# Kernel optimization log

Measured on AMD Instinct MI355X. Metric: run time of the kernel, lower is better.

## Reference

```python
import jax, jax.numpy as jnp
import numpy as np

N_NODES = 10000
N_EDGES = 80000
IN_DIM = 512
H1, H2, OUT_DIM = 4096, 1024, 7
NEG_SLOPE = 0.2


def _gat_layer(x, src, dst, W, a_src, a_dst, b, n_nodes):
    # x: [N, F_in] -> h: [N, F_out]
    h = x @ W
    # per-edge attention logits: a_src . h_i + a_dst . h_j (PyG GATConv, heads=1)
    e = jax.nn.leaky_relu((h @ a_src)[src] + (h @ a_dst)[dst], NEG_SLOPE)
    # segment softmax over destination nodes
    m = jax.ops.segment_max(e, dst, num_segments=n_nodes)
    ex = jnp.exp(e - m[dst])
    denom = jax.ops.segment_sum(ex, dst, num_segments=n_nodes)
    alpha = ex / denom[dst]
    # scatter-add weighted messages
    out = jax.ops.segment_sum(alpha[:, None] * h[src], dst, num_segments=n_nodes)
    return out + b


def setup_inputs() -> dict:
    key = jax.random.key(0)
    ks = jax.random.split(key, 16)
    s = 0.05
    inp = {
        "x": jax.random.normal(ks[0], (N_NODES, IN_DIM), dtype=jnp.float32),
        "edge_index": jax.random.randint(ks[1], (2, N_EDGES), 0, N_NODES, dtype=jnp.int32),
        "W1": jax.random.normal(ks[2], (IN_DIM, H1), dtype=jnp.float32) * s,
        "att_src1": jax.random.normal(ks[3], (H1,), dtype=jnp.float32) * s,
        "att_dst1": jax.random.normal(ks[4], (H1,), dtype=jnp.float32) * s,
        "b1": jnp.zeros((H1,), dtype=jnp.float32),
        "W2": jax.random.normal(ks[5], (H1, H2), dtype=jnp.float32) * s,
        "att_src2": jax.random.normal(ks[6], (H2,), dtype=jnp.float32) * s,
        "att_dst2": jax.random.normal(ks[7], (H2,), dtype=jnp.float32) * s,
        "b2": jnp.zeros((H2,), dtype=jnp.float32),
        "W3": jax.random.normal(ks[8], (H2, OUT_DIM), dtype=jnp.float32) * s,
        "att_src3": jax.random.normal(ks[9], (OUT_DIM,), dtype=jnp.float32) * s,
        "att_dst3": jax.random.normal(ks[10], (OUT_DIM,), dtype=jnp.float32) * s,
        "b3": jnp.zeros((OUT_DIM,), dtype=jnp.float32),
    }
    return inp


def reference(x, edge_index, W1, att_src1, att_dst1, b1,
              W2, att_src2, att_dst2, b2,
              W3, att_src3, att_dst3, b3):
    n = x.shape[0]
    loops = jnp.arange(n, dtype=edge_index.dtype)
    src = jnp.concatenate([edge_index[0], loops])  # add_self_loops=True
    dst = jnp.concatenate([edge_index[1], loops])
    h = _gat_layer(x, src, dst, W1, att_src1, att_dst1, b1, n)
    h = jax.nn.relu(h)  # dropout is identity in eval mode
    h = _gat_layer(h, src, dst, W2, att_src2, att_dst2, b2, n)
    h = jax.nn.relu(h)
    h = _gat_layer(h, src, dst, W3, att_src3, att_dst3, b3, n)
    return jax.nn.log_softmax(h, axis=1)
```

## Files before the change

kernel.cpp:

```cpp
#include <hip/hip_runtime.h>
#include <hip/hip_bf16.h>
#include <math.h>

#define NNODES  10000
#define NEDGES  80000
#define NTOT    90000
#define IN_DIM  512
#define H1_DIM  4096
#define H2_DIM  1024
#define ODIM    7
#define MAXDEG  128
#define NEG_SLOPE 0.2f

typedef __hip_bfloat16 bf16;
typedef __attribute__((ext_vector_type(8))) short short8;
typedef __attribute__((ext_vector_type(4))) float f32x4;

__device__ inline void unpack_bf2(unsigned u, float& lo, float& hi) {
    union { unsigned i; float f; } a, b;
    a.i = u << 16; b.i = u & 0xffff0000u;
    lo = a.f; hi = b.f;
}

#define ASYNC_COPY16(lds, g)                                                              \
    __builtin_amdgcn_global_load_lds((const __attribute__((address_space(1))) void*)(g),  \
                                     (__attribute__((address_space(3))) void*)(lds),      \
                                     16, 0, 0)

__global__ void build_bucket(const int* __restrict__ ei, int* cnt, int* bucket) {
    int k = blockIdx.x * blockDim.x + threadIdx.x;
    if (k >= NTOT) return;
    int s, d;
    if (k < NEDGES) { s = ei[k]; d = ei[NEDGES + k]; }
    else            { s = k - NEDGES; d = s; }
    int pos = atomicAdd(&cnt[d], 1);
    if (pos < MAXDEG) bucket[d * MAXDEG + pos] = s;
}

__global__ __launch_bounds__(256) void transpose_fold(const float* __restrict__ W,
                                                      bf16* __restrict__ WT,
                                                      const float* __restrict__ a_s,
                                                      const float* __restrict__ a_d,
                                                      float* __restrict__ w_s,
                                                      float* __restrict__ w_d,
                                                      int R, int C) {
    __shared__ float t[32][33];
    int c0 = blockIdx.x * 32, r0 = blockIdx.y * 32;
    int x = threadIdx.x & 31, y = threadIdx.x >> 5;
    float asv = a_s[c0 + x], adv = a_d[c0 + x];
    #pragma unroll
    for (int dy = 0; dy < 32; dy += 8) {
        float w = W[(size_t)(r0 + y + dy) * C + c0 + x];
        t[y + dy][x] = w;
        float ps = w * asv, pd = w * adv;
        #pragma unroll
        for (int off = 16; off > 0; off >>= 1) {
            ps += __shfl_down(ps, off, 32);
            pd += __shfl_down(pd, off, 32);
        }
        if (x == 0) {
            atomicAdd(&w_s[r0 + y + dy], ps);
            atomicAdd(&w_d[r0 + y + dy], pd);
        }
    }
    __syncthreads();
    #pragma unroll
    for (int dy = 0; dy < 32; dy += 8)
        WT[(size_t)(c0 + y + dy) * R + r0 + x] = __float2bfloat16(t[x][y + dy]);
}

__global__ __launch_bounds__(128) void dots_cvt1(const float* __restrict__ X,
                                                 const float* __restrict__ w_s,
                                                 const float* __restrict__ w_d,
                                                 float* __restrict__ s_src,
                                                 float* __restrict__ s_dst,
                                                 bf16* __restrict__ XB) {
    int n = blockIdx.x;
    int t = threadIdx.x;
    float4 xv = ((const float4*)(X + (size_t)n * IN_DIM))[t];
    float4 wsv = ((const float4*)w_s)[t];
    float4 wdv = ((const float4*)w_d)[t];
    bf16 o[4] = { __float2bfloat16(xv.x), __float2bfloat16(xv.y),
                  __float2bfloat16(xv.z), __float2bfloat16(xv.w) };
    *(uint2*)(XB + (size_t)n * IN_DIM + 4 * t) = *(uint2*)o;
    float ss = xv.x*wsv.x + xv.y*wsv.y + xv.z*wsv.z + xv.w*wsv.w;
    float sd = xv.x*wdv.x + xv.y*wdv.y + xv.z*wdv.z + xv.w*wdv.w;
    #pragma unroll
    for (int off = 32; off > 0; off >>= 1) {
        ss += __shfl_down(ss, off);
        sd += __shfl_down(sd, off);
    }
    __shared__ float red[2][2];
    int wave = t >> 6;
    if ((t & 63) == 0) { red[0][wave] = ss; red[1][wave] = sd; }
    __syncthreads();
    if (t == 0) {
        s_src[n] = red[0][0] + red[0][1];
        s_dst[n] = red[1][0] + red[1][1];
    }
}

__global__ __launch_bounds__(128) void agg1(const bf16* __restrict__ XB,
                                            const float* __restrict__ s_src,
                                            const float* __restrict__ s_dst,
                                            const int* __restrict__ bucket,
                                            const int* __restrict__ cnt,
                                            bf16* __restrict__ OUT) {
    int n = blockIdx.x;
    int c = min(cnt[n], MAXDEG);
    __shared__ float alpha[MAXDEG];
    __shared__ int   ssrc[MAXDEG];
    if (threadIdx.x < c) {
        int s = bucket[n * MAXDEG + threadIdx.x];
        ssrc[threadIdx.x] = s;
        float e = s_src[s] + s_dst[n];
        alpha[threadIdx.x] = (e > 0.f) ? e : NEG_SLOPE * e;
    }
    __syncthreads();
    if (threadIdx.x == 0) {
        float m = -1e30f;
        for (int j = 0; j < c; ++j) m = fmaxf(m, alpha[j]);
        float s = 0.f;
        for (int j = 0; j < c; ++j) { float ex = __expf(alpha[j] - m); alpha[j] = ex; s += ex; }
        float inv = 1.f / s;
        for (int j = 0; j < c; ++j) alpha[j] *= inv;
    }
    __syncthreads();
    int t = threadIdx.x;
    float acc[4] = {};
    for (int j = 0; j < c; ++j) {
        float a = alpha[j];
        uint2 raw = ((const uint2*)(XB + (size_t)ssrc[j] * IN_DIM))[t];
        float f0, f1, f2, f3;
        unpack_bf2(raw.x, f0, f1); unpack_bf2(raw.y, f2, f3);
        acc[0] = fmaf(a, f0, acc[0]); acc[1] = fmaf(a, f1, acc[1]);
        acc[2] = fmaf(a, f2, acc[2]); acc[3] = fmaf(a, f3, acc[3]);
    }
    bf16 o[4] = { __float2bfloat16(acc[0]), __float2bfloat16(acc[1]),
                  __float2bfloat16(acc[2]), __float2bfloat16(acc[3]) };
    *(uint2*)(OUT + (size_t)n * IN_DIM + 4 * t) = *(uint2*)o;
}

__global__ __launch_bounds__(128) void agg2_h3(const bf16* __restrict__ H,
                                               const float* __restrict__ s_src,
                                               const float* __restrict__ s_dst,
                                               const int* __restrict__ bucket,
                                               const int* __restrict__ cnt,
                                               const float* __restrict__ bias,
                                               const float* __restrict__ W3,
                                               const float* __restrict__ as3,
                                               const float* __restrict__ ad3,
                                               float* __restrict__ H3,
                                               float* __restrict__ s3_src,
                                               float* __restrict__ s3_dst) {
    int n = blockIdx.x;
    int c = min(cnt[n], MAXDEG);
    __shared__ float alpha[MAXDEG];
    __shared__ int   ssrc[MAXDEG];
    if (threadIdx.x < c) {
        int s = bucket[n * MAXDEG + threadIdx.x];
        ssrc[threadIdx.x] = s;
        float e = s_src[s] + s_dst[n];
        alpha[threadIdx.x] = (e > 0.f) ? e : NEG_SLOPE * e;
    }
    __syncthreads();
    if (threadIdx.x == 0) {
        float m = -1e30f;
        for (int j = 0; j < c; ++j) m = fmaxf(m, alpha[j]);
        float s = 0.f;
        for (int j = 0; j < c; ++j) { float ex = __expf(alpha[j] - m); alpha[j] = ex; s += ex; }
        float inv = 1.f / s;
        for (int j = 0; j < c; ++j) alpha[j] *= inv;
    }
    __syncthreads();
    int t = threadIdx.x;
    float acc[8] = {};
    for (int j = 0; j < c; ++j) {
        float a = alpha[j];
        uint4 raw = ((const uint4*)(H + (size_t)ssrc[j] * H2_DIM))[t];
        float f0, f1, f2, f3, f4, f5, f6, f7;
        unpack_bf2(raw.x, f0, f1); unpack_bf2(raw.y, f2, f3);
        unpack_bf2(raw.z, f4, f5); unpack_bf2(raw.w, f6, f7);
        acc[0] = fmaf(a, f0, acc[0]); acc[1] = fmaf(a, f1, acc[1]);
        acc[2] = fmaf(a, f2, acc[2]); acc[3] = fmaf(a, f3, acc[3]);
        acc[4] = fmaf(a, f4, acc[4]); acc[5] = fmaf(a, f5, acc[5]);
        acc[6] = fmaf(a, f6, acc[6]); acc[7] = fmaf(a, f7, acc[7]);
    }
    float p[ODIM] = {};
    #pragma unroll
    for (int k = 0; k < 8; ++k) {
        float v = fmaxf(acc[k] + bias[8 * t + k], 0.f);
        const float* wrow = W3 + (size_t)(8 * t + k) * ODIM;
        #pragma unroll
        for (int o = 0; o < ODIM; ++o)
            p[o] = fmaf(v, wrow[o], p[o]);
    }
    #pragma unroll
    for (int o = 0; o < ODIM; ++o)
        #pragma unroll
        for (int off = 32; off > 0; off >>= 1)
            p[o] += __shfl_down(p[o], off);
    __shared__ float red[2][ODIM];
    int wave = t >> 6;
    if ((t & 63) == 0)
        #pragma unroll
        for (int o = 0; o < ODIM; ++o) red[wave][o] = p[o];
    __syncthreads();
    if (t == 0) {
        float ss = 0.f, sd = 0.f;
        #pragma unroll
        for (int o = 0; o < ODIM; ++o) {
            float v = red[0][o] + red[1][o];
            H3[n * ODIM + o] = v;
            ss = fmaf(v, as3[o], ss);
            sd = fmaf(v, ad3[o], sd);
        }
        s3_src[n] = ss; s3_dst[n] = sd;
    }
}

template<int TM, int TN, bool BIASRELU, bool FUSEDOTS>
__global__ __launch_bounds__(256) void gemm_mfma(const bf16* __restrict__ A,
                                                 const bf16* __restrict__ BT,
                                                 const float* __restrict__ bias,
                                                 const float* __restrict__ w_s,
                                                 const float* __restrict__ w_d,
                                                 float* __restrict__ s_src,
                                                 float* __restrict__ s_dst,
                                                 bf16* __restrict__ C,
                                                 int M, int N, int K) {
    constexpr int NI = TM / 32;
    constexpr int NJ = TN / 32;
    __shared__ alignas(16) bf16 As[2][TM][32];
    __shared__ alignas(16) bf16 Bs[2][TN][32];
    const int tid  = threadIdx.x;
    const int wave = tid >> 6;
    const int lane = tid & 63;

    const int gx = gridDim.x;
    const int j  = blockIdx.y * gx + blockIdx.x;
    const int band = j / (8 * gx);
    const int r8   = j - band * (8 * gx);
    const int by = (r8 & 7) + 8 * band;
    const int bx = r8 >> 3;
    const int row0 = by * TM;
    const int col0 = bx * TN;
    if (row0 >= M) return;

    const int wr0 = (wave >> 1) * (TM / 2);
    const int wc0 = (wave & 1) * (TN / 2);

    const int srow  = tid >> 2;
    const int skoff = ((tid & 3) ^ (srow & 3)) * 8;
    const bf16* a0 = A + (size_t)min(row0 + srow, M - 1) * K + skoff;
    const bf16* a1 = A + (size_t)min(row0 + 64 + srow, M - 1) * K + skoff;
    const bf16* b0 = BT + (size_t)(col0 + srow) * K + skoff;
    const bf16* b1 = BT + (size_t)(col0 + 64 + srow) * K + skoff;

    f32x4 acc[NI][NJ] = {};
    const int fRow  = lane & 15;
    const int fKoff = ((lane >> 4) ^ (fRow & 3)) * 8;

    const int NIT = K >> 5;
    ASYNC_COPY16(&As[0][wave * 16][0],      a0);
    ASYNC_COPY16(&As[0][64 + wave * 16][0], a1);
    ASYNC_COPY16(&Bs[0][wave * 16][0],      b0);
    ASYNC_COPY16(&Bs[0][64 + wave * 16][0], b1);
    __syncthreads();

    for (int it = 0; it < NIT; ++it) {
        const int cb = it & 1, nb = cb ^ 1;
        if (it + 1 < NIT) {
            const int ko = (it + 1) << 5;
            ASYNC_COPY16(&As[nb][wave * 16][0],      a0 + ko);
            ASYNC_COPY16(&As[nb][64 + wave * 16][0], a1 + ko);
            ASYNC_COPY16(&Bs[nb][wave * 16][0],      b0 + ko);
            ASYNC_COPY16(&Bs[nb][64 + wave * 16][0], b1 + ko);
        }
        short8 af[NI], bfr[NJ];
        #pragma unroll
        for (int i = 0; i < NI; ++i)
            af[i] = *(const short8*)&As[cb][wr0 + i * 16 + fRow][fKoff];
        #pragma unroll
        for (int jj = 0; jj < NJ; ++jj)
            bfr[jj] = *(const short8*)&Bs[cb][wc0 + jj * 16 + fRow][fKoff];
        #pragma unroll
        for (int i = 0; i < NI; ++i)
            #pragma unroll
            for (int jj = 0; jj < NJ; ++jj)
                acc[i][jj] = __builtin_amdgcn_mfma_f32_16x16x32_bf16(af[i], bfr[jj], acc[i][jj], 0, 0, 0);
        __syncthreads();
    }

    const int crow = (lane >> 4) * 4;
    const int ccol = lane & 15;
    #pragma unroll
    for (int i = 0; i < NI; ++i) {
        #pragma unroll
        for (int r = 0; r < 4; ++r) {
            int gm = row0 + wr0 + i * 16 + crow + r;
            float vss = 0.f, vsd = 0.f;
            if (gm < M) {
                #pragma unroll
                for (int jj = 0; jj < NJ; ++jj) {
                    int gn = col0 + wc0 + jj * 16 + ccol;
                    float v = acc[i][jj][r];
                    if (BIASRELU) v = fmaxf(v + bias[gn], 0.f);
                    C[(size_t)gm * N + gn] = __float2bfloat16(v);
                    if (FUSEDOTS) {
                        vss = fmaf(v, w_s[gn], vss);
                        vsd = fmaf(v, w_d[gn], vsd);
                    }
                }
            }
            if (FUSEDOTS) {
                #pragma unroll
                for (int m2 = 1; m2 < 16; m2 <<= 1) {
                    vss += __shfl_xor(vss, m2, 16);
                    vsd += __shfl_xor(vsd, m2, 16);
                }
                if ((lane & 15) == 0 && gm < M) {
                    atomicAdd(&s_src[gm], vss);
                    atomicAdd(&s_dst[gm], vsd);
                }
            }
        }
    }
}

__global__ __launch_bounds__(128) void aggregate3(const float* __restrict__ H3,
                                                  const float* __restrict__ s_src,
                                                  const float* __restrict__ s_dst,
                                                  const int* __restrict__ bucket,
                                                  const int* __restrict__ cnt,
                                                  const float* __restrict__ b3,
                                                  float* __restrict__ out) {
    int n = blockIdx.x;
    int c = min(cnt[n], MAXDEG);
    __shared__ float alpha[MAXDEG];
    __shared__ int   ssrc[MAXDEG];
    __shared__ float o[ODIM];
    if (threadIdx.x < c) {
        int s = bucket[n * MAXDEG + threadIdx.x];
        ssrc[threadIdx.x] = s;
        float e = s_src[s] + s_dst[n];
        alpha[threadIdx.x] = (e > 0.f) ? e : NEG_SLOPE * e;
    }
    __syncthreads();
    if (threadIdx.x == 0) {
        float m = -1e30f;
        for (int j = 0; j < c; ++j) m = fmaxf(m, alpha[j]);
        float s = 0.f;
        for (int j = 0; j < c; ++j) { float ex = __expf(alpha[j] - m); alpha[j] = ex; s += ex; }
        float inv = 1.f / s;
        for (int j = 0; j < c; ++j) alpha[j] *= inv;
    }
    __syncthreads();
    if (threadIdx.x < ODIM) {
        float acc = 0.f;
        for (int j = 0; j < c; ++j)
            acc = fmaf(alpha[j], H3[ssrc[j] * ODIM + threadIdx.x], acc);
        o[threadIdx.x] = acc + b3[threadIdx.x];
    }
    __syncthreads();
    if (threadIdx.x == 0) {
        float m = o[0];
        for (int k = 1; k < ODIM; ++k) m = fmaxf(m, o[k]);
        float s = 0.f;
        for (int k = 0; k < ODIM; ++k) s += __expf(o[k] - m);
        float lse = m + logf(s);
        for (int k = 0; k < ODIM; ++k) out[n * ODIM + k] = o[k] - lse;
    }
}

extern "C" void kernel_launch(void* const* d_in, const int* in_sizes, int n_in,
                              void* d_out, int out_size, void* d_ws, size_t ws_size,
                              hipStream_t stream) {
    const float* x   = (const float*)d_in[0];
    const int*   ei  = (const int*)  d_in[1];
    const float* W1  = (const float*)d_in[2];
    const float* as1 = (const float*)d_in[3];
    const float* ad1 = (const float*)d_in[4];
    const float* b1  = (const float*)d_in[5];
    const float* W2  = (const float*)d_in[6];
    const float* as2 = (const float*)d_in[7];
    const float* ad2 = (const float*)d_in[8];
    const float* b2  = (const float*)d_in[9];
    const float* W3  = (const float*)d_in[10];
    const float* as3 = (const float*)d_in[11];
    const float* ad3 = (const float*)d_in[12];
    const float* b3  = (const float*)d_in[13];
    float* outp = (float*)d_out;

    char* p = (char*)d_ws;
    bf16*  x2     = (bf16*)p;   p += (size_t)NNODES * H1_DIM * sizeof(bf16);
    bf16*  r2     = (bf16*)p;   p += (size_t)NNODES * H2_DIM * sizeof(bf16);
    bf16*  r3     = (bf16*)p;   p += (size_t)NNODES * H2_DIM * sizeof(bf16);
    bf16*  W2T    = (bf16*)p;   p += (size_t)H2_DIM * H1_DIM * sizeof(bf16);
    float* h3     = (float*)p;  p += (size_t)NNODES * ODIM * sizeof(float);
    float* ssrc   = (float*)p;  p += NNODES * sizeof(float);
    float* sdst   = (float*)p;  p += NNODES * sizeof(float);
    float* ssrc3  = (float*)p;  p += NNODES * sizeof(float);
    float* sdst3  = (float*)p;  p += NNODES * sizeof(float);
    float* w1s    = (float*)p;  p += IN_DIM * sizeof(float);
    float* w1d    = (float*)p;  p += IN_DIM * sizeof(float);
    float* w2s    = (float*)p;  p += H1_DIM * sizeof(float);
    float* w2d    = (float*)p;  p += H1_DIM * sizeof(float);
    int*   cnt    = (int*)p;    p += NNODES * sizeof(int);
    int*   bucket = (int*)p;    p += (size_t)NNODES * MAXDEG * sizeof(int);
    size_t required = (size_t)(p - (char*)d_ws);
    if (ws_size < required) return;

    bf16* xb    = x2;
    bf16* aggxb = r2;
    bf16* h2    = r2;
    bf16* W1T   = r3;

    hipMemsetAsync(cnt, 0, NNODES * sizeof(int), stream);
    hipMemsetAsync(w1s, 0, (2 * IN_DIM + 2 * H1_DIM) * sizeof(float), stream);
    build_bucket<<<(NTOT + 255) / 256, 256, 0, stream>>>(ei, cnt, bucket);

    {
        dim3 tg1(H1_DIM / 32, IN_DIM / 32);
        transpose_fold<<<tg1, 256, 0, stream>>>(W1, W1T, as1, ad1, w1s, w1d, IN_DIM, H1_DIM);
        dim3 tg2(H2_DIM / 32, H1_DIM / 32);
        transpose_fold<<<tg2, 256, 0, stream>>>(W2, W2T, as2, ad2, w2s, w2d, H1_DIM, H2_DIM);
    }

    dots_cvt1<<<NNODES, 128, 0, stream>>>(x, w1s, w1d, ssrc, sdst, xb);
    agg1<<<NNODES, 128, 0, stream>>>(xb, ssrc, sdst, bucket, cnt, aggxb);

    const int nRowPad = ((((NNODES + 127) / 128) + 7) / 8) * 8;

    hipMemsetAsync(ssrc, 0, 2 * NNODES * sizeof(float), stream);
    {
        dim3 g(H1_DIM / 128, nRowPad);
        gemm_mfma<128, 128, true, true><<<g, 256, 0, stream>>>(aggxb, W1T, b1, w2s, w2d,
                                                               ssrc, sdst, x2, NNODES, H1_DIM, IN_DIM);
    }

    {
        dim3 g(H2_DIM / 128, nRowPad);
        gemm_mfma<128, 128, false, false><<<g, 256, 0, stream>>>(x2, W2T, nullptr, nullptr, nullptr,
                                                                 nullptr, nullptr, h2, NNODES, H2_DIM, H1_DIM);
    }

    agg2_h3<<<NNODES, 128, 0, stream>>>(h2, ssrc, sdst, bucket, cnt, b2,
                                        W3, as3, ad3, h3, ssrc3, sdst3);

    aggregate3<<<NNODES, 128, 0, stream>>>(h3, ssrc3, sdst3, bucket, cnt, b3, outp);
}
```

Baseline: 440.1 us.

## Switch GEMMs to 32x32x16 MFMA tiles and merge weight transpose launches

Replaces the 16x16x32 bf16 MFMA fragments with 32x32x16 fragments, so each wave computes a 64x64 tile from a 2x2 set of 16-float accumulators, with a new epilogue row mapping and a 32-lane reduction for the fused attention dots. Adds a non-pipelined variant for the first GEMM (K=512) that loads two 32-wide K slices per barrier, and keeps double buffering for the second GEMM. Merges the two transpose_fold launches into one kernel. The larger MFMA shape is meant to cut LDS fragment reads per FLOP, at the cost of different register pressure and a new swizzled read pattern that has to match the existing store swizzle.

```diff
diff --git a/kernel.cpp b/kernel.cpp
--- a/kernel.cpp
+++ b/kernel.cpp
@@ -14,7 +14,7 @@
 
 typedef __hip_bfloat16 bf16;
 typedef __attribute__((ext_vector_type(8))) short short8;
-typedef __attribute__((ext_vector_type(4))) float f32x4;
+typedef __attribute__((ext_vector_type(16))) float f32x16;
 
 __device__ inline void unpack_bf2(unsigned u, float& lo, float& hi) {
     union { unsigned i; float f; } a, b;
@@ -37,15 +37,28 @@
     if (pos < MAXDEG) bucket[d * MAXDEG + pos] = s;
 }
 
-__global__ __launch_bounds__(256) void transpose_fold(const float* __restrict__ W,
-                                                      bf16* __restrict__ WT,
-                                                      const float* __restrict__ a_s,
-                                                      const float* __restrict__ a_d,
-                                                      float* __restrict__ w_s,
-                                                      float* __restrict__ w_d,
-                                                      int R, int C) {
+__global__ __launch_bounds__(256) void transpose_fold2(const float* __restrict__ W1,
+                                                       bf16* __restrict__ W1T,
+                                                       const float* __restrict__ as1,
+                                                       const float* __restrict__ ad1,
+                                                       float* __restrict__ w1s,
+                                                       float* __restrict__ w1d,
+                                                       const float* __restrict__ W2,
+                                                       bf16* __restrict__ W2T,
+                                                       const float* __restrict__ as2,
+                                                       const float* __restrict__ ad2,
+                                                       float* __restrict__ w2s,
+                                                       float* __restrict__ w2d) {
+    const int nb1 = (H1_DIM / 32) * (IN_DIM / 32);
+    int bid = blockIdx.x;
+    const float *W, *a_s, *a_d; bf16 *WT; float *w_s, *w_d; int R, C, cblocks;
+    if (bid < nb1) { W = W1; WT = W1T; a_s = as1; a_d = ad1; w_s = w1s; w_d = w1d;
+                     R = IN_DIM; C = H1_DIM; cblocks = H1_DIM / 32; }
+    else { bid -= nb1; W = W2; WT = W2T; a_s = as2; a_d = ad2; w_s = w2s; w_d = w2d;
+           R = H1_DIM; C = H2_DIM; cblocks = H2_DIM / 32; }
+    int c0 = (bid % cblocks) * 32, r0 = (bid / cblocks) * 32;
+
     __shared__ float t[32][33];
-    int c0 = blockIdx.x * 32, r0 = blockIdx.y * 32;
     int x = threadIdx.x & 31, y = threadIdx.x >> 5;
     float asv = a_s[c0 + x], adv = a_d[c0 + x];
     #pragma unroll
@@ -219,7 +232,7 @@
     }
 }
 
-template<int TM, int TN, bool BIASRELU, bool FUSEDOTS>
+template<bool BIASRELU, bool FUSEDOTS, bool PIPE>
 __global__ __launch_bounds__(256) void gemm_mfma(const bf16* __restrict__ A,
                                                  const bf16* __restrict__ BT,
                                                  const float* __restrict__ bias,
@@ -229,8 +242,7 @@
                                                  float* __restrict__ s_dst,
                                                  bf16* __restrict__ C,
                                                  int M, int N, int K) {
-    constexpr int NI = TM / 32;
-    constexpr int NJ = TN / 32;
+    constexpr int TM = 128, TN = 128;
     __shared__ alignas(16) bf16 As[2][TM][32];
     __shared__ alignas(16) bf16 Bs[2][TN][32];
     const int tid  = threadIdx.x;
@@ -247,8 +259,8 @@
     const int col0 = bx * TN;
     if (row0 >= M) return;
 
-    const int wr0 = (wave >> 1) * (TM / 2);
-    const int wc0 = (wave & 1) * (TN / 2);
+    const int wr0 = (wave >> 1) * 64;
+    const int wc0 = (wave & 1) * 64;
 
     const int srow  = tid >> 2;
     const int skoff = ((tid & 3) ^ (srow & 3)) * 8;
@@ -257,54 +269,82 @@
     const bf16* b0 = BT + (size_t)(col0 + srow) * K + skoff;
     const bf16* b1 = BT + (size_t)(col0 + 64 + srow) * K + skoff;
 
-    f32x4 acc[NI][NJ] = {};
-    const int fRow  = lane & 15;
-    const int fKoff = ((lane >> 4) ^ (fRow & 3)) * 8;
-
-    const int NIT = K >> 5;
-    ASYNC_COPY16(&As[0][wave * 16][0],      a0);
-    ASYNC_COPY16(&As[0][64 + wave * 16][0], a1);
-    ASYNC_COPY16(&Bs[0][wave * 16][0],      b0);
-    ASYNC_COPY16(&Bs[0][64 + wave * 16][0], b1);
-    __syncthreads();
-
-    for (int it = 0; it < NIT; ++it) {
-        const int cb = it & 1, nb = cb ^ 1;
-        if (it + 1 < NIT) {
-            const int ko = (it + 1) << 5;
-            ASYNC_COPY16(&As[nb][wave * 16][0],      a0 + ko);
-            ASYNC_COPY16(&As[nb][64 + wave * 16][0], a1 + ko);
-            ASYNC_COPY16(&Bs[nb][wave * 16][0],      b0 + ko);
-            ASYNC_COPY16(&Bs[nb][64 + wave * 16][0], b1 + ko);
-        }
-        short8 af[NI], bfr[NJ];
-        #pragma unroll
-        for (int i = 0; i < NI; ++i)
-            af[i] = *(const short8*)&As[cb][wr0 + i * 16 + fRow][fKoff];
-        #pragma unroll
-        for (int jj = 0; jj < NJ; ++jj)
-            bfr[jj] = *(const short8*)&Bs[cb][wc0 + jj * 16 + fRow][fKoff];
-        #pragma unroll
-        for (int i = 0; i < NI; ++i)
+    f32x16 acc[2][2] = {};
+    const int frow   = lane & 31;
+    const int chunkb = lane >> 5;
+    const int cswz   = lane & 3;
+
+    #define MFMA_STEP(buf, ks)                                                             \
+        {                                                                                  \
+            short8 af[2], bfr[2];                                                          \
+            const int pc = ((((ks) << 1) | chunkb) ^ cswz) * 8;                            \
+            _Pragma("unroll")                                                              \
+            for (int fi = 0; fi < 2; ++fi)                                                 \
+                af[fi] = *(const short8*)&As[buf][wr0 + fi * 32 + frow][pc];               \
+            _Pragma("unroll")                                                              \
+            for (int fj = 0; fj < 2; ++fj)                                                 \
+                bfr[fj] = *(const short8*)&Bs[buf][wc0 + fj * 32 + frow][pc];              \
+            _Pragma("unroll")                                                              \
+            for (int fi = 0; fi < 2; ++fi)                                                 \
+                _Pragma("unroll")                                                          \
+                for (int fj = 0; fj < 2; ++fj)                                             \
+                    acc[fi][fj] = __builtin_amdgcn_mfma_f32_32x32x16_bf16(                 \
+                        af[fi], bfr[fj], acc[fi][fj], 0, 0, 0);                            \
+        }
+
+    if constexpr (PIPE) {
+        const int NIT = K >> 5;
+        ASYNC_COPY16(&As[0][wave * 16][0],      a0);
+        ASYNC_COPY16(&As[0][64 + wave * 16][0], a1);
+        ASYNC_COPY16(&Bs[0][wave * 16][0],      b0);
+        ASYNC_COPY16(&Bs[0][64 + wave * 16][0], b1);
+        __syncthreads();
+        for (int it = 0; it < NIT; ++it) {
+            const int cb = it & 1, nb = cb ^ 1;
+            if (it + 1 < NIT) {
+                const int ko = (it + 1) << 5;
+                ASYNC_COPY16(&As[nb][wave * 16][0],      a0 + ko);
+                ASYNC_COPY16(&As[nb][64 + wave * 16][0], a1 + ko);
+                ASYNC_COPY16(&Bs[nb][wave * 16][0],      b0 + ko);
+                ASYNC_COPY16(&Bs[nb][64 + wave * 16][0], b1 + ko);
+            }
+            MFMA_STEP(cb, 0)
+            MFMA_STEP(cb, 1)
+            __syncthreads();
+        }
+    } else {
+        for (int k0 = 0; k0 < K; k0 += 64) {
             #pragma unroll
-            for (int jj = 0; jj < NJ; ++jj)
-                acc[i][jj] = __builtin_amdgcn_mfma_f32_16x16x32_bf16(af[i], bfr[jj], acc[i][jj], 0, 0, 0);
-        __syncthreads();
-    }
-
-    const int crow = (lane >> 4) * 4;
-    const int ccol = lane & 15;
-    #pragma unroll
-    for (int i = 0; i < NI; ++i) {
-        #pragma unroll
-        for (int r = 0; r < 4; ++r) {
-            int gm = row0 + wr0 + i * 16 + crow + r;
+            for (int h = 0; h < 2; ++h) {
+                ASYNC_COPY16(&As[h][wave * 16][0],      a0 + k0 + h * 32);
+                ASYNC_COPY16(&As[h][64 + wave * 16][0], a1 + k0 + h * 32);
+                ASYNC_COPY16(&Bs[h][wave * 16][0],      b0 + k0 + h * 32);
+                ASYNC_COPY16(&Bs[h][64 + wave * 16][0], b1 + k0 + h * 32);
+            }
+            __syncthreads();
+            MFMA_STEP(0, 0)
+            MFMA_STEP(0, 1)
+            MFMA_STEP(1, 0)
+            MFMA_STEP(1, 1)
+            __syncthreads();
+        }
+    }
+    #undef MFMA_STEP
+
+    const int halfsel = lane >> 5;
+    const int ccol = lane & 31;
+    #pragma unroll
+    for (int fi = 0; fi < 2; ++fi) {
+        #pragma unroll
+        for (int r = 0; r < 16; ++r) {
+            const int rowin = (r & 3) + 8 * (r >> 2) + 4 * halfsel;
+            int gm = row0 + wr0 + fi * 32 + rowin;
             float vss = 0.f, vsd = 0.f;
             if (gm < M) {
                 #pragma unroll
-                for (int jj = 0; jj < NJ; ++jj) {
-                    int gn = col0 + wc0 + jj * 16 + ccol;
-                    float v = acc[i][jj][r];
+                for (int fj = 0; fj < 2; ++fj) {
+                    int gn = col0 + wc0 + fj * 32 + ccol;
+                    float v = acc[fi][fj][r];
                     if (BIASRELU) v = fmaxf(v + bias[gn], 0.f);
                     C[(size_t)gm * N + gn] = __float2bfloat16(v);
                     if (FUSEDOTS) {
@@ -315,11 +355,11 @@
             }
             if (FUSEDOTS) {
                 #pragma unroll
-                for (int m2 = 1; m2 < 16; m2 <<= 1) {
-                    vss += __shfl_xor(vss, m2, 16);
-                    vsd += __shfl_xor(vsd, m2, 16);
+                for (int m2 = 1; m2 < 32; m2 <<= 1) {
+                    vss += __shfl_xor(vss, m2, 32);
+                    vsd += __shfl_xor(vsd, m2, 32);
                 }
-                if ((lane & 15) == 0 && gm < M) {
+                if (ccol == 0 && gm < M) {
                     atomicAdd(&s_src[gm], vss);
                     atomicAdd(&s_dst[gm], vsd);
                 }
@@ -421,10 +461,10 @@
     build_bucket<<<(NTOT + 255) / 256, 256, 0, stream>>>(ei, cnt, bucket);
 
     {
-        dim3 tg1(H1_DIM / 32, IN_DIM / 32);
-        transpose_fold<<<tg1, 256, 0, stream>>>(W1, W1T, as1, ad1, w1s, w1d, IN_DIM, H1_DIM);
-        dim3 tg2(H2_DIM / 32, H1_DIM / 32);
-        transpose_fold<<<tg2, 256, 0, stream>>>(W2, W2T, as2, ad2, w2s, w2d, H1_DIM, H2_DIM);
+        int nb1 = (H1_DIM / 32) * (IN_DIM / 32);
+        int nb2 = (H2_DIM / 32) * (H1_DIM / 32);
+        transpose_fold2<<<nb1 + nb2, 256, 0, stream>>>(W1, W1T, as1, ad1, w1s, w1d,
+                                                       W2, W2T, as2, ad2, w2s, w2d);
     }
 
     dots_cvt1<<<NNODES, 128, 0, stream>>>(x, w1s, w1d, ssrc, sdst, xb);
@@ -435,14 +475,14 @@
     hipMemsetAsync(ssrc, 0, 2 * NNODES * sizeof(float), stream);
     {
         dim3 g(H1_DIM / 128, nRowPad);
-        gemm_mfma<128, 128, true, true><<<g, 256, 0, stream>>>(aggxb, W1T, b1, w2s, w2d,
-                                                               ssrc, sdst, x2, NNODES, H1_DIM, IN_DIM);
+        gemm_mfma<true, true, false><<<g, 256, 0, stream>>>(aggxb, W1T, b1, w2s, w2d,
+                                                            ssrc, sdst, x2, NNODES, H1_DIM, IN_DIM);
     }
 
     {
         dim3 g(H2_DIM / 128, nRowPad);
-        gemm_mfma<128, 128, false, false><<<g, 256, 0, stream>>>(x2, W2T, nullptr, nullptr, nullptr,
-                                                                 nullptr, nullptr, h2, NNODES, H2_DIM, H1_DIM);
+        gemm_mfma<false, false, true><<<g, 256, 0, stream>>>(x2, W2T, nullptr, nullptr, nullptr,
+                                                             nullptr, nullptr, h2, NNODES, H2_DIM, H1_DIM);
     }
 
     agg2_h3<<<NNODES, 128, 0, stream>>>(h2, ssrc, sdst, bucket, cnt, b2,
```

New measurement: 506.5 us. +15.1%, slower.
